# Kernel optimization log

Measured on AMD Instinct MI355X. Metric: run time of the kernel, lower is better.

## Reference

```python
import jax, jax.numpy as jnp
import numpy as np
import math

B, S, H = 2, 2048, 2048
NH, NKV, HD = 16, 4, 128


def _rope_tables(seq_len, head_dim):
    # Standard RoPE: freqs over half dim, duplicated to full head_dim.
    inv_freq = 1.0 / (10000.0 ** (np.arange(0, head_dim, 2, dtype=np.float32) / head_dim))
    t = np.arange(seq_len, dtype=np.float32)
    freqs = np.outer(t, inv_freq)  # [S, HD/2]
    emb = np.concatenate([freqs, freqs], axis=-1)  # [S, HD]
    return jnp.asarray(np.cos(emb)), jnp.asarray(np.sin(emb))


def setup_inputs() -> dict:
    key = jax.random.key(0)
    k1, k2, k3, k4 = jax.random.split(key, 4)
    cos, sin = _rope_tables(S, HD)
    return {
        "x": jax.random.normal(k1, (B, S, H), dtype=jnp.float32),
        "cos": cos,
        "sin": sin,
        "Wq": jax.random.normal(k2, (H, NH * HD), dtype=jnp.float32) * (1.0 / math.sqrt(H)),
        "Wkv": jax.random.normal(k3, (H, 2 * NKV * HD), dtype=jnp.float32) * (1.0 / math.sqrt(H)),
        "Wo": jax.random.normal(k4, (NH * HD, H), dtype=jnp.float32) * (1.0 / math.sqrt(NH * HD)),
    }


def _rotate_half(x):
    x1, x2 = jnp.split(x, 2, axis=-1)
    return jnp.concatenate([-x2, x1], axis=-1)


def _apply_rotary(x, cos, sin):
    # x: [B, S, nheads, HD]; cos/sin: [S, HD]
    c = cos[None, :, None, :]
    s = sin[None, :, None, :]
    return x * c + _rotate_half(x) * s


def reference(x, cos, sin, Wq, Wkv, Wo):
    b, s, _ = x.shape
    q = (x @ Wq).reshape(b, s, NH, HD)
    kv = x @ Wkv
    k, v = jnp.split(kv, [NKV * HD], axis=-1)
    k = k.reshape(b, s, NKV, HD)
    v = v.reshape(b, s, NKV, HD)
    q = _apply_rotary(q, cos, sin)
    k = _apply_rotary(k, cos, sin)
    # to [B, heads, S, HD]
    q = jnp.transpose(q, (0, 2, 1, 3))
    k = jnp.transpose(k, (0, 2, 1, 3))
    v = jnp.transpose(v, (0, 2, 1, 3))
    # GQA: repeat K/V heads
    rep = NH // NKV
    k = jnp.repeat(k, rep, axis=1)
    v = jnp.repeat(v, rep, axis=1)
    scale = jnp.asarray(1.0 / math.sqrt(HD), dtype=x.dtype)
    scores = jnp.einsum('bhqd,bhkd->bhqk', q * scale, k)  # [B, NH, S, S]
    causal = jnp.tril(jnp.ones((s, s), dtype=jnp.bool_))
    scores = jnp.where(causal, scores, jnp.asarray(-jnp.inf, scores.dtype))
    attn = jax.nn.softmax(scores, axis=-1)
    out = jnp.einsum('bhqk,bhkd->bhqd', attn, v)
    out = jnp.transpose(out, (0, 2, 1, 3)).reshape(b, s, NH * HD)
    return out @ Wo
```

## Files before the change

### kernel.cpp

```cpp
#include <hip/hip_runtime.h>
#include <math.h>

#define NB 2
#define SEQ 2048
#define HDIM 2048
#define NHD 16
#define NKVH 4
#define HEADD 128
#define MROWS (NB*SEQ)
#define NQCOLS (NHD*HEADD)
#define QKVCOLS 3072

typedef unsigned short ushortT;
typedef __attribute__((ext_vector_type(8))) short short8;
typedef __attribute__((ext_vector_type(4))) float floatx4;
typedef __attribute__((ext_vector_type(4))) unsigned short ushort4v;

__device__ __forceinline__ ushortT f2bf(float f) {
  union { float f; unsigned int u; } v; v.f = f;
  unsigned int r = v.u + 0x7FFFu + ((v.u >> 16) & 1u);
  return (ushortT)(r >> 16);
}
__device__ __forceinline__ float bf2f(ushortT u) {
  union { unsigned int u; float f; } v; v.u = ((unsigned int)u) << 16;
  return v.f;
}

__device__ __forceinline__ void gload16(const ushortT* g, ushortT* l) {
  __builtin_amdgcn_global_load_lds(
      (const __attribute__((address_space(1))) void*)g,
      (__attribute__((address_space(3))) void*)l, 16, 0, 0);
}

__global__ __launch_bounds__(256) void cast_bf16_kernel(
    const float* __restrict__ in, ushortT* __restrict__ out, int n4) {
  int i = blockIdx.x * 256 + threadIdx.x;
  if (i >= n4) return;
  float4 v = ((const float4*)in)[i];
  ushort4v o;
  o.x = f2bf(v.x); o.y = f2bf(v.y); o.z = f2bf(v.z); o.w = f2bf(v.w);
  ((ushort4v*)out)[i] = o;
}

__global__ __launch_bounds__(256) void transpose_cast_kernel(
    const float* __restrict__ in, ushortT* __restrict__ out, int R, int C) {
  __shared__ ushortT tile[32][33];
  int c0 = blockIdx.x * 32, r0 = blockIdx.y * 32;
  int tx = threadIdx.x & 31, ty = threadIdx.x >> 5;
#pragma unroll
  for (int i = 0; i < 4; ++i)
    tile[ty + i*8][tx] = f2bf(in[(size_t)(r0 + ty + i*8) * C + c0 + tx]);
  __syncthreads();
#pragma unroll
  for (int i = 0; i < 4; ++i)
    out[(size_t)(c0 + ty + i*8) * R + r0 + tx] = tile[tx][ty + i*8];
}

__global__ __launch_bounds__(256) void gemm_bt_kernel(
    const ushortT* __restrict__ A, const ushortT* __restrict__ Bt,
    void* __restrict__ C, int M, int N, int K, int c_fp32) {
  __shared__ __align__(16) ushortT lA[128 * 64];
  __shared__ __align__(16) ushortT lB[128 * 64];
  const int m0 = blockIdx.y * 128;
  const int n0 = blockIdx.x * 128;
  const int tid = threadIdx.x;
  const int wave = tid >> 6, lane = tid & 63;
  const int g = lane >> 4, l15 = lane & 15;
  const int wm = (wave >> 1) * 64, wn = (wave & 1) * 64;
  const int sw = l15 & 7;

  floatx4 acc[4][4] = {};

  for (int kt = 0; kt < K; kt += 64) {
    __syncthreads();
#pragma unroll
    for (int i = 0; i < 4; ++i) {
      int s = i * 256 + tid;
      int r = s >> 3, j = s & 7;
      int col8 = j ^ (r & 7);
      gload16(A  + (size_t)(m0 + r) * K + kt + col8 * 8, lA + s * 8);
      gload16(Bt + (size_t)(n0 + r) * K + kt + col8 * 8, lB + s * 8);
    }
    __syncthreads();
#pragma unroll
    for (int ks = 0; ks < 2; ++ks) {
      short8 af[4], bfv[4];
#pragma unroll
      for (int t = 0; t < 4; ++t) {
        af[t]  = *(const short8*)(lA + (wm + t * 16 + l15) * 64 + ((ks * 4 + g) ^ sw) * 8);
        bfv[t] = *(const short8*)(lB + (wn + t * 16 + l15) * 64 + ((ks * 4 + g) ^ sw) * 8);
      }
#pragma unroll
      for (int mt = 0; mt < 4; ++mt)
#pragma unroll
        for (int nt = 0; nt < 4; ++nt)
          acc[mt][nt] = __builtin_amdgcn_mfma_f32_16x16x32_bf16(
              af[mt], bfv[nt], acc[mt][nt], 0, 0, 0);
    }
  }

#pragma unroll
  for (int mt = 0; mt < 4; ++mt)
#pragma unroll
    for (int nt = 0; nt < 4; ++nt)
#pragma unroll
      for (int r = 0; r < 4; ++r) {
        int row = m0 + wm + mt * 16 + g * 4 + r;
        int col = n0 + wn + nt * 16 + l15;
        float v = acc[mt][nt][r];
        if (c_fp32) ((float*)C)[(size_t)row * N + col] = v;
        else ((ushortT*)C)[(size_t)row * N + col] = f2bf(v);
      }
}

__global__ __launch_bounds__(256) void rope_q_kernel(
    const ushortT* __restrict__ QKVtmp, const float* __restrict__ cosT,
    const float* __restrict__ sinT, ushortT* __restrict__ Qr) {
  int idx = blockIdx.x * 256 + threadIdx.x;
  int d = idx & 63;
  int t = idx >> 6;
  int h = t & (NHD - 1);
  int bs = t >> 4;
  int s = bs & (SEQ - 1);
  int b = bs >> 11;
  float c = cosT[s * HEADD + d], sn = sinT[s * HEADD + d];
  float q1 = bf2f(QKVtmp[(size_t)bs * QKVCOLS + h * HEADD + d]);
  float q2 = bf2f(QKVtmp[(size_t)bs * QKVCOLS + h * HEADD + d + 64]);
  size_t o = ((size_t)(b * NHD + h) * SEQ + s) * HEADD + d;
  Qr[o]      = f2bf(q1 * c - q2 * sn);
  Qr[o + 64] = f2bf(q2 * c + q1 * sn);
}

__global__ __launch_bounds__(256) void rope_k_kernel(
    const ushortT* __restrict__ QKVtmp, const float* __restrict__ cosT,
    const float* __restrict__ sinT, ushortT* __restrict__ Kr) {
  int idx = blockIdx.x * 256 + threadIdx.x;
  int d = idx & 63;
  int t = idx >> 6;
  int kvh = t & (NKVH - 1);
  int bs = t >> 2;
  int s = bs & (SEQ - 1);
  int b = bs >> 11;
  float c = cosT[s * HEADD + d], sn = sinT[s * HEADD + d];
  float k1 = bf2f(QKVtmp[(size_t)bs * QKVCOLS + 2048 + kvh * HEADD + d]);
  float k2 = bf2f(QKVtmp[(size_t)bs * QKVCOLS + 2048 + kvh * HEADD + d + 64]);
  size_t o = ((size_t)(b * NKVH + kvh) * SEQ + s) * HEADD + d;
  Kr[o]      = f2bf(k1 * c - k2 * sn);
  Kr[o + 64] = f2bf(k2 * c + k1 * sn);
}

__global__ __launch_bounds__(256) void v_relayout_kernel(
    const ushortT* __restrict__ QKVtmp, ushortT* __restrict__ Vt) {
  __shared__ ushortT tile[32][33];
  int bk = blockIdx.z;
  int b = bk >> 2, kvh = bk & 3;
  int s0 = blockIdx.x * 32, d0 = blockIdx.y * 32;
  int tx = threadIdx.x & 31, ty = threadIdx.x >> 5;
#pragma unroll
  for (int i = 0; i < 4; ++i) {
    int s = s0 + ty + i * 8;
    tile[ty + i * 8][tx] =
        QKVtmp[(size_t)(b * SEQ + s) * QKVCOLS + 2560 + kvh * HEADD + d0 + tx];
  }
  __syncthreads();
#pragma unroll
  for (int i = 0; i < 4; ++i) {
    int d = d0 + ty + i * 8;
    Vt[((size_t)bk * HEADD + d) * SEQ + s0 + tx] = tile[tx][ty + i * 8];
  }
}

__global__ __launch_bounds__(256) void attn_kernel(
    const ushortT* __restrict__ Q,
    const ushortT* __restrict__ Kg,
    const ushortT* __restrict__ Vg,
    ushortT* __restrict__ Oa) {
  __shared__ __align__(16) ushortT lK[64 * 128];
  __shared__ __align__(16) ushortT lV[128 * 64];
  __shared__ __align__(16) ushortT lP[4 * 32 * 72];

  const int tid = threadIdx.x;
  const int w = tid >> 6, lane = tid & 63;
  const int g = lane >> 4, l15 = lane & 15;
  const int sw = l15 & 7;
  const int bh = blockIdx.x;
  const int b = bh >> 4, h = bh & 15;
  const int kvh = h >> 2;
  const int yi = blockIdx.y;
  const int qi = (yi < 8) ? (15 - yi) : (yi - 8);
  const int q0 = qi << 7;
  const int qw = q0 + w * 32;

  const float SC = 0.08838834764831845f * 1.4426950408889634f;

  short8 qf[2][4];
#pragma unroll
  for (int mt = 0; mt < 2; ++mt) {
    const ushortT* qp =
        Q + (((size_t)(b * NHD + h)) * SEQ + qw + mt * 16 + l15) * HEADD + g * 8;
#pragma unroll
    for (int ks = 0; ks < 4; ++ks) qf[mt][ks] = *(const short8*)(qp + ks * 32);
  }

  floatx4 o[2][8] = {};
  float m_s[2] = {-INFINITY, -INFINITY};
  float l_s[2] = {0.f, 0.f};

  const ushortT* kbase = Kg + ((size_t)(b * NKVH + kvh)) * SEQ * HEADD;
  const ushortT* vbase = Vg + ((size_t)(b * NKVH + kvh)) * HEADD * SEQ;
  ushortT* pw = lP + w * 32 * 72;

  const int nkt = 2 * qi + 2;
  for (int kt = 0; kt < nkt; ++kt) {
    __syncthreads();
#pragma unroll
    for (int ii = 0; ii < 4; ++ii) {
      int s = ii * 256 + tid;
      int r = s >> 4, j = (s & 15) ^ (r & 7);
      gload16(kbase + (size_t)(kt * 64 + r) * HEADD + j * 8, lK + s * 8);
    }
#pragma unroll
    for (int ii = 0; ii < 4; ++ii) {
      int s = ii * 256 + tid;
      int r = s >> 3, j = (s & 7) ^ (r & 7);
      gload16(vbase + (size_t)r * SEQ + kt * 64 + j * 8, lV + s * 8);
    }
    __syncthreads();

    if (kt == nkt - 1 && w < 2) continue;

    floatx4 sc[2][4] = {};
#pragma unroll
    for (int ks = 0; ks < 4; ++ks)
#pragma unroll
      for (int nt = 0; nt < 4; ++nt) {
        short8 kf = *(const short8*)(lK + (nt * 16 + l15) * 128 + ((ks * 4 + g) ^ sw) * 8);
        sc[0][nt] = __builtin_amdgcn_mfma_f32_16x16x32_bf16(kf, qf[0][ks], sc[0][nt], 0, 0, 0);
        sc[1][nt] = __builtin_amdgcn_mfma_f32_16x16x32_bf16(kf, qf[1][ks], sc[1][nt], 0, 0, 0);
      }

#pragma unroll
    for (int mt = 0; mt < 2; ++mt) {
      const int qsub = qw + mt * 16;
      const bool needmask = (kt * 64 + 63) > qsub;
      float ps[4][4];
      float mx = -INFINITY;
#pragma unroll
      for (int nt = 0; nt < 4; ++nt)
#pragma unroll
        for (int r = 0; r < 4; ++r) {
          float v = sc[mt][nt][r] * SC;
          if (needmask) {
            int kg = kt * 64 + nt * 16 + g * 4 + r;
            if (kg > qsub + l15) v = -INFINITY;
          }
          ps[nt][r] = v;
          mx = fmaxf(mx, v);
        }
      mx = fmaxf(mx, __shfl_xor(mx, 16));
      mx = fmaxf(mx, __shfl_xor(mx, 32));
      float mn = fmaxf(m_s[mt], mx);
      float alpha = __builtin_amdgcn_exp2f(m_s[mt] - mn);
      m_s[mt] = mn;
      float rs = 0.f;
#pragma unroll
      for (int nt = 0; nt < 4; ++nt) {
        ushort4v pk;
#pragma unroll
        for (int r = 0; r < 4; ++r) {
          float e = __builtin_amdgcn_exp2f(ps[nt][r] - mn);
          rs += e;
          ((ushortT*)&pk)[r] = f2bf(e);
        }
        *(ushort4v*)(pw + (mt * 16 + l15) * 72 + nt * 16 + g * 4) = pk;
      }
      rs += __shfl_xor(rs, 16);
      rs += __shfl_xor(rs, 32);
      l_s[mt] = l_s[mt] * alpha + rs;
#pragma unroll
      for (int dt = 0; dt < 8; ++dt)
#pragma unroll
        for (int r = 0; r < 4; ++r) o[mt][dt][r] *= alpha;
    }

#pragma unroll
    for (int ks = 0; ks < 2; ++ks) {
      short8 bp0 = *(const short8*)(pw + (0 * 16 + l15) * 72 + ks * 32 + g * 8);
      short8 bp1 = *(const short8*)(pw + (1 * 16 + l15) * 72 + ks * 32 + g * 8);
#pragma unroll
      for (int dt = 0; dt < 8; ++dt) {
        short8 vf = *(const short8*)(lV + (dt * 16 + l15) * 64 + ((ks * 4 + g) ^ sw) * 8);
        o[0][dt] = __builtin_amdgcn_mfma_f32_16x16x32_bf16(vf, bp0, o[0][dt], 0, 0, 0);
        o[1][dt] = __builtin_amdgcn_mfma_f32_16x16x32_bf16(vf, bp1, o[1][dt], 0, 0, 0);
      }
    }
  }

#pragma unroll
  for (int mt = 0; mt < 2; ++mt) {
    float inv = 1.f / l_s[mt];
    int qg = qw + mt * 16 + l15;
#pragma unroll
    for (int dt = 0; dt < 8; ++dt) {
      ushort4v ov;
#pragma unroll
      for (int r = 0; r < 4; ++r) ((ushortT*)&ov)[r] = f2bf(o[mt][dt][r] * inv);
      *(ushort4v*)(Oa + (size_t)(b * SEQ + qg) * NQCOLS + h * HEADD + dt * 16 + g * 4) = ov;
    }
  }
}

extern "C" void kernel_launch(void* const* d_in, const int* in_sizes, int n_in,
                              void* d_out, int out_size, void* d_ws, size_t ws_size,
                              hipStream_t stream) {
  const float* x    = (const float*)d_in[0];
  const float* cosT = (const float*)d_in[1];
  const float* sinT = (const float*)d_in[2];
  const float* Wq   = (const float*)d_in[3];
  const float* Wkv  = (const float*)d_in[4];
  const float* Wo   = (const float*)d_in[5];

  char* ws = (char*)d_ws;
  ushortT* x_bf   = (ushortT*)(ws + 0);
  ushortT* Wqkvt  = (ushortT*)(ws + 16777216);
  ushortT* Wot    = (ushortT*)(ws + 29360128);
  ushortT* QKVtmp = (ushortT*)(ws + 37748736);
  ushortT* Qr     = (ushortT*)(ws + 62914560);
  ushortT* Kr     = (ushortT*)(ws + 79691776);
  ushortT* Vt     = (ushortT*)(ws + 83886080);
  ushortT* Oattn  = QKVtmp;

  cast_bf16_kernel<<<8192, 256, 0, stream>>>(x, x_bf, (MROWS * HDIM) / 4);
  transpose_cast_kernel<<<dim3(64, 64), 256, 0, stream>>>(Wq, Wqkvt, HDIM, NQCOLS);
  transpose_cast_kernel<<<dim3(32, 64), 256, 0, stream>>>(Wkv, Wqkvt + 2048 * 2048, HDIM, 1024);
  transpose_cast_kernel<<<dim3(64, 64), 256, 0, stream>>>(Wo, Wot, NQCOLS, HDIM);

  gemm_bt_kernel<<<dim3(24, 32), 256, 0, stream>>>(x_bf, Wqkvt, QKVtmp, MROWS, QKVCOLS, HDIM, 0);

  rope_q_kernel<<<16384, 256, 0, stream>>>(QKVtmp, cosT, sinT, Qr);
  rope_k_kernel<<<4096, 256, 0, stream>>>(QKVtmp, cosT, sinT, Kr);
  v_relayout_kernel<<<dim3(64, 4, 8), 256, 0, stream>>>(QKVtmp, Vt);

  attn_kernel<<<dim3(32, 16), 256, 0, stream>>>(Qr, Kr, Vt, Oattn);

  gemm_bt_kernel<<<dim3(16, 32), 256, 0, stream>>>(Oattn, Wot, d_out, MROWS, HDIM, NQCOLS, 1);
}
```

Baseline: 376.0 us.

## Read K/V fragments directly from global memory instead of staging in LDS

Removes the cooperative LDS staging of K and V tiles and the two block-wide barriers per key tile; each wave now loads its MFMA K and V fragments straight from global memory (relying on L1/L2 reuse across the four waves sharing a KV head). The per-wave loop count is also adjusted so waves skip the last tile without participating in loads, and launch bounds request 2 blocks per CU. This trades LDS traffic and synchronization for redundant global/cache loads, which may increase memory latency exposure in the inner loop.

```diff
diff --git a/kernel.cpp b/kernel.cpp
--- a/kernel.cpp
+++ b/kernel.cpp
@@ -170,19 +170,16 @@
   }
 }
 
-__global__ __launch_bounds__(256) void attn_kernel(
+__global__ __launch_bounds__(256, 2) void attn_kernel(
     const ushortT* __restrict__ Q,
     const ushortT* __restrict__ Kg,
     const ushortT* __restrict__ Vg,
     ushortT* __restrict__ Oa) {
-  __shared__ __align__(16) ushortT lK[64 * 128];
-  __shared__ __align__(16) ushortT lV[128 * 64];
   __shared__ __align__(16) ushortT lP[4 * 32 * 72];
 
   const int tid = threadIdx.x;
   const int w = tid >> 6, lane = tid & 63;
   const int g = lane >> 4, l15 = lane & 15;
-  const int sw = l15 & 7;
   const int bh = blockIdx.x;
   const int b = bh >> 4, h = bh & 15;
   const int kvh = h >> 2;
@@ -210,31 +207,15 @@
   const ushortT* vbase = Vg + ((size_t)(b * NKVH + kvh)) * HEADD * SEQ;
   ushortT* pw = lP + w * 32 * 72;
 
-  const int nkt = 2 * qi + 2;
+  const int nkt = 2 * qi + 2 - (w < 2 ? 1 : 0);
   for (int kt = 0; kt < nkt; ++kt) {
-    __syncthreads();
-#pragma unroll
-    for (int ii = 0; ii < 4; ++ii) {
-      int s = ii * 256 + tid;
-      int r = s >> 4, j = (s & 15) ^ (r & 7);
-      gload16(kbase + (size_t)(kt * 64 + r) * HEADD + j * 8, lK + s * 8);
-    }
-#pragma unroll
-    for (int ii = 0; ii < 4; ++ii) {
-      int s = ii * 256 + tid;
-      int r = s >> 3, j = (s & 7) ^ (r & 7);
-      gload16(vbase + (size_t)r * SEQ + kt * 64 + j * 8, lV + s * 8);
-    }
-    __syncthreads();
-
-    if (kt == nkt - 1 && w < 2) continue;
-
+    const ushortT* kp = kbase + (size_t)kt * 64 * HEADD;
     floatx4 sc[2][4] = {};
 #pragma unroll
     for (int ks = 0; ks < 4; ++ks)
 #pragma unroll
       for (int nt = 0; nt < 4; ++nt) {
-        short8 kf = *(const short8*)(lK + (nt * 16 + l15) * 128 + ((ks * 4 + g) ^ sw) * 8);
+        short8 kf = *(const short8*)(kp + (size_t)(nt * 16 + l15) * HEADD + ks * 32 + g * 8);
         sc[0][nt] = __builtin_amdgcn_mfma_f32_16x16x32_bf16(kf, qf[0][ks], sc[0][nt], 0, 0, 0);
         sc[1][nt] = __builtin_amdgcn_mfma_f32_16x16x32_bf16(kf, qf[1][ks], sc[1][nt], 0, 0, 0);
       }
@@ -285,11 +266,12 @@
 
 #pragma unroll
     for (int ks = 0; ks < 2; ++ks) {
-      short8 bp0 = *(const short8*)(pw + (0 * 16 + l15) * 72 + ks * 32 + g * 8);
-      short8 bp1 = *(const short8*)(pw + (1 * 16 + l15) * 72 + ks * 32 + g * 8);
+      short8 bp0 = *(const short8*)(pw + l15 * 72 + ks * 32 + g * 8);
+      short8 bp1 = *(const short8*)(pw + (16 + l15) * 72 + ks * 32 + g * 8);
 #pragma unroll
       for (int dt = 0; dt < 8; ++dt) {
-        short8 vf = *(const short8*)(lV + (dt * 16 + l15) * 64 + ((ks * 4 + g) ^ sw) * 8);
+        short8 vf = *(const short8*)(vbase + (size_t)(dt * 16 + l15) * SEQ +
+                                     kt * 64 + ks * 32 + g * 8);
         o[0][dt] = __builtin_amdgcn_mfma_f32_16x16x32_bf16(vf, bp0, o[0][dt], 0, 0, 0);
         o[1][dt] = __builtin_amdgcn_mfma_f32_16x16x32_bf16(vf, bp1, o[1][dt], 0, 0, 0);
       }
```

Measured after the change: 403.6 us. 7.3% more time.

## Split long causal attention query tiles across two KV chunks with merge kernel

Applied to the files above, without the earlier changes.

For query tiles 8-15, which have the most KV tiles under causal masking, the KV loop is split into two chunks of at most 16 tiles, each handled by its own block. Each block writes fp32 partial outputs and running max/sum to workspace, and a new merge kernel combines them with log-sum-exp weights. This balances per-block work and raises the grid from 512 to 768 blocks to shorten the tail, at the cost of extra partial-result traffic, reused workspace regions, and one more kernel launch.

```diff
diff --git a/kernel.cpp b/kernel.cpp
--- a/kernel.cpp
+++ b/kernel.cpp
@@ -170,11 +170,18 @@
   }
 }
 
+__device__ __constant__ const signed char QI_TAB[24] =
+    {8,9,10,11,12,13,14,7, 15,15,6,14,5,13,4,12, 0,8,1,9,2,10,3,11};
+__device__ __constant__ const signed char CH_TAB[24] =
+    {0,0,0,0,0,0,0,0, 0,1,0,1,0,1,0,1, 0,1,0,1,0,1,0,1};
+
 __global__ __launch_bounds__(256) void attn_kernel(
     const ushortT* __restrict__ Q,
     const ushortT* __restrict__ Kg,
     const ushortT* __restrict__ Vg,
-    ushortT* __restrict__ Oa) {
+    ushortT* __restrict__ Oa,
+    float* __restrict__ PartA, float* __restrict__ PartB,
+    float* __restrict__ Ml) {
   __shared__ __align__(16) ushortT lK[64 * 128];
   __shared__ __align__(16) ushortT lV[128 * 64];
   __shared__ __align__(16) ushortT lP[4 * 32 * 72];
@@ -186,8 +193,8 @@
   const int bh = blockIdx.x;
   const int b = bh >> 4, h = bh & 15;
   const int kvh = h >> 2;
-  const int yi = blockIdx.y;
-  const int qi = (yi < 8) ? (15 - yi) : (yi - 8);
+  const int qi = QI_TAB[blockIdx.y];
+  const int ch = CH_TAB[blockIdx.y];
   const int q0 = qi << 7;
   const int qw = q0 + w * 32;
 
@@ -210,8 +217,10 @@
   const ushortT* vbase = Vg + ((size_t)(b * NKVH + kvh)) * HEADD * SEQ;
   ushortT* pw = lP + w * 32 * 72;
 
-  const int nkt = 2 * qi + 2;
-  for (int kt = 0; kt < nkt; ++kt) {
+  const int ktend = 2 * qi + 2;
+  const int kt0 = ch * 16;
+  const int kt1 = (ktend < kt0 + 16) ? ktend : (kt0 + 16);
+  for (int kt = kt0; kt < kt1; ++kt) {
     __syncthreads();
 #pragma unroll
     for (int ii = 0; ii < 4; ++ii) {
@@ -227,7 +236,7 @@
     }
     __syncthreads();
 
-    if (kt == nkt - 1 && w < 2) continue;
+    if (kt == ktend - 1 && w < 2) continue;
 
     floatx4 sc[2][4] = {};
 #pragma unroll
@@ -285,8 +294,8 @@
 
 #pragma unroll
     for (int ks = 0; ks < 2; ++ks) {
-      short8 bp0 = *(const short8*)(pw + (0 * 16 + l15) * 72 + ks * 32 + g * 8);
-      short8 bp1 = *(const short8*)(pw + (1 * 16 + l15) * 72 + ks * 32 + g * 8);
+      short8 bp0 = *(const short8*)(pw + l15 * 72 + ks * 32 + g * 8);
+      short8 bp1 = *(const short8*)(pw + (16 + l15) * 72 + ks * 32 + g * 8);
 #pragma unroll
       for (int dt = 0; dt < 8; ++dt) {
         short8 vf = *(const short8*)(lV + (dt * 16 + l15) * 64 + ((ks * 4 + g) ^ sw) * 8);
@@ -296,17 +305,67 @@
     }
   }
 
-#pragma unroll
-  for (int mt = 0; mt < 2; ++mt) {
-    float inv = 1.f / l_s[mt];
-    int qg = qw + mt * 16 + l15;
-#pragma unroll
-    for (int dt = 0; dt < 8; ++dt) {
-      ushort4v ov;
-#pragma unroll
-      for (int r = 0; r < 4; ++r) ((ushortT*)&ov)[r] = f2bf(o[mt][dt][r] * inv);
-      *(ushort4v*)(Oa + (size_t)(b * SEQ + qg) * NQCOLS + h * HEADD + dt * 16 + g * 4) = ov;
-    }
+  if (qi < 8) {
+#pragma unroll
+    for (int mt = 0; mt < 2; ++mt) {
+      float inv = 1.f / l_s[mt];
+      int qg = qw + mt * 16 + l15;
+#pragma unroll
+      for (int dt = 0; dt < 8; ++dt) {
+        ushort4v ov;
+#pragma unroll
+        for (int r = 0; r < 4; ++r) ((ushortT*)&ov)[r] = f2bf(o[mt][dt][r] * inv);
+        *(ushort4v*)(Oa + (size_t)(b * SEQ + qg) * NQCOLS + h * HEADD + dt * 16 + g * 4) = ov;
+      }
+    }
+  } else {
+    int p = (bh * 8 + (qi - 8)) * 2 + ch;
+    float* Pp = (p < 448) ? (PartA + (size_t)p * 16384)
+                          : (PartB + (size_t)(p - 448) * 16384);
+    float* mlp = Ml + p * 256;
+#pragma unroll
+    for (int mt = 0; mt < 2; ++mt) {
+      int ql = w * 32 + mt * 16 + l15;
+      if (g == 0) { mlp[ql * 2] = m_s[mt]; mlp[ql * 2 + 1] = l_s[mt]; }
+#pragma unroll
+      for (int dt = 0; dt < 8; ++dt)
+        *(floatx4*)(Pp + ql * 128 + dt * 16 + g * 4) = o[mt][dt];
+    }
+  }
+}
+
+__global__ __launch_bounds__(256) void attn_merge_kernel(
+    const float* __restrict__ PartA, const float* __restrict__ PartB,
+    const float* __restrict__ Ml, ushortT* __restrict__ Oa) {
+  int bh = blockIdx.x, qih = blockIdx.y;
+  int b = bh >> 4, h = bh & 15;
+  int p0 = (bh * 8 + qih) * 2, p1 = p0 + 1;
+  const float* P0 = (p0 < 448) ? (PartA + (size_t)p0 * 16384)
+                               : (PartB + (size_t)(p0 - 448) * 16384);
+  const float* P1 = (p1 < 448) ? (PartA + (size_t)p1 * 16384)
+                               : (PartB + (size_t)(p1 - 448) * 16384);
+  int row = threadIdx.x >> 1, dh = (threadIdx.x & 1) * 64;
+  float m0 = Ml[p0 * 256 + row * 2], l0 = Ml[p0 * 256 + row * 2 + 1];
+  float m1 = Ml[p1 * 256 + row * 2], l1 = Ml[p1 * 256 + row * 2 + 1];
+  float mm = fmaxf(m0, m1);
+  float w0 = __builtin_amdgcn_exp2f(m0 - mm);
+  float w1 = __builtin_amdgcn_exp2f(m1 - mm);
+  float inv = 1.f / (w0 * l0 + w1 * l1);
+  w0 *= inv; w1 *= inv;
+  int q = (8 + qih) * 128 + row;
+  ushortT* op = Oa + (size_t)(b * SEQ + q) * NQCOLS + h * HEADD + dh;
+  const float* a = P0 + row * 128 + dh;
+  const float* c = P1 + row * 128 + dh;
+#pragma unroll
+  for (int d = 0; d < 64; d += 4) {
+    float4 va = *(const float4*)(a + d);
+    float4 vc = *(const float4*)(c + d);
+    ushort4v ov;
+    ov.x = f2bf(w0 * va.x + w1 * vc.x);
+    ov.y = f2bf(w0 * va.y + w1 * vc.y);
+    ov.z = f2bf(w0 * va.z + w1 * vc.z);
+    ov.w = f2bf(w0 * va.w + w1 * vc.w);
+    *(ushort4v*)(op + d) = ov;
   }
 }
 
@@ -329,6 +388,9 @@
   ushortT* Kr     = (ushortT*)(ws + 79691776);
   ushortT* Vt     = (ushortT*)(ws + 83886080);
   ushortT* Oattn  = QKVtmp;
+  float* PartA = (float*)(ws + 0);
+  float* PartB = (float*)(ws + 54525952);
+  float* Ml    = (float*)(ws + 58720256);
 
   cast_bf16_kernel<<<8192, 256, 0, stream>>>(x, x_bf, (MROWS * HDIM) / 4);
   transpose_cast_kernel<<<dim3(64, 64), 256, 0, stream>>>(Wq, Wqkvt, HDIM, NQCOLS);
@@ -341,7 +403,8 @@
   rope_k_kernel<<<4096, 256, 0, stream>>>(QKVtmp, cosT, sinT, Kr);
   v_relayout_kernel<<<dim3(64, 4, 8), 256, 0, stream>>>(QKVtmp, Vt);
 
-  attn_kernel<<<dim3(32, 16), 256, 0, stream>>>(Qr, Kr, Vt, Oattn);
+  attn_kernel<<<dim3(32, 24), 256, 0, stream>>>(Qr, Kr, Vt, Oattn, PartA, PartB, Ml);
+  attn_merge_kernel<<<dim3(32, 8), 256, 0, stream>>>(PartA, PartB, Ml, Oattn);
 
   gemm_bt_kernel<<<dim3(16, 32), 256, 0, stream>>>(Oattn, Wot, d_out, MROWS, HDIM, NQCOLS, 1);
 }
```

Result: slower. 401.8 us (+6.8%).
